# Kernel optimization log

Measured on AMD Instinct MI355X. Metric: run time of the kernel, lower is better.

Reference implementation:

```python
import jax, jax.numpy as jnp
import numpy as np

B, N, DIM, H = 8, 4096, 1024, 16
D = DIM // H
EPS_NORM = 1e-12
EPS_PI = 1e-8


def setup_inputs() -> dict:
    key = jax.random.key(0)
    k1, k2, k3 = jax.random.split(key, 3)
    x = jax.random.normal(k1, (B, N, DIM), dtype=jnp.float32)
    Wqkv = jax.random.normal(k2, (DIM, DIM), dtype=jnp.float32) * (1.0 / np.sqrt(DIM))
    temp = jnp.ones((H, 1), dtype=jnp.float32)
    Wout = jax.random.normal(k3, (DIM, DIM), dtype=jnp.float32) * (1.0 / np.sqrt(DIM))
    bout = jnp.zeros((DIM,), dtype=jnp.float32)
    return {"x": x, "Wqkv": Wqkv, "temp": temp, "Wout": Wout, "bout": bout}


def reference(x, Wqkv, temp, Wout, bout):
    b, n, dim = x.shape
    h, d = H, dim // H
    # qkv linear (no bias), then 'b n (h d) -> b h n d'
    w = (x @ Wqkv.T).reshape(b, n, h, d).transpose(0, 2, 1, 3)  # (b,h,N,d)
    # F.normalize along the sequence axis (dim=-2)
    norm = jnp.sqrt(jnp.sum(w * w, axis=-2, keepdims=True))
    w_normed = w / jnp.maximum(norm, EPS_NORM)
    # logits (b,h,N); temp (h,1) broadcasts over N. Softmax over dim=1 (heads).
    logits = jnp.sum(w_normed * w_normed, axis=-1) * temp[None, :, :]
    Pi = jax.nn.softmax(logits, axis=1)  # (b,h,N)
    Pi_norm = Pi / (jnp.sum(Pi, axis=-1, keepdims=True) + EPS_PI)
    # dots: (b,h,1,N) @ (b,h,N,d) -> (b,h,d)
    dots = jnp.einsum('bhn,bhnd->bhd', Pi_norm, w * w)
    attn = 1.0 / (1.0 + dots)  # (b,h,d)
    out = -(w * Pi[..., None]) * attn[:, :, None, :]  # (b,h,N,d)
    out = out.transpose(0, 2, 1, 3).reshape(b, n, dim)  # 'b h n d -> b n (h d)'
    return out @ Wout.T + bout
```

## Files before the change

### kernel.cpp

```cpp
#include <hip/hip_runtime.h>
#include <stdint.h>
#include <math.h>

#define B_ 8
#define N_ 4096
#define DIM_ 1024
#define H_ 16
#define M_ (B_*N_)

typedef unsigned short u16;
typedef __attribute__((ext_vector_type(8))) short bf16x8;
typedef __attribute__((ext_vector_type(4))) float f32x4;

__device__ __forceinline__ u16 f2bf(float f) {
    union { float f; uint32_t u; } c; c.f = f;
    uint32_t r = (c.u + 0x7fffu + ((c.u >> 16) & 1u)) >> 16;
    return (u16)r;
}
__device__ __forceinline__ float bf2f(u16 u) {
    union { uint32_t u; float f; } c; c.u = ((uint32_t)u) << 16;
    return c.f;
}
__device__ __forceinline__ void gload_lds16(const void* g, void* l) {
    __builtin_amdgcn_global_load_lds(
        (const __attribute__((address_space(1))) uint32_t*)g,
        (__attribute__((address_space(3))) uint32_t*)l, 16, 0, 0);
}

template<int MODE>
__global__ __launch_bounds__(512)
void gemm_mfma(const u16* __restrict__ Ah,
               const u16* __restrict__ Bh, const u16* __restrict__ Bl,
               const float* __restrict__ bias, float* __restrict__ Cf,
               float* __restrict__ norm2)
{
    __shared__ u16 sAh[256*32], sBh[128*32], sBl[128*32];
    __shared__ float cs[128];
    const int tid  = threadIdx.x;
    const int wid  = tid >> 6;
    const int lane = tid & 63;
    const int bid = blockIdx.x;
    const int lin = (bid & 7) * 128 + (bid >> 3);
    const int bx = lin & 7;
    const int by = lin >> 3;
    const int wm = wid >> 1, wn = wid & 1;
    const int fr = lane & 15;
    const int kb = (lane >> 4) * 8;

    f32x4 acc[4][4] = {};

    const int arow = by * 256;
    const int brow = bx * 128;

    for (int k0 = 0; k0 < DIM_; k0 += 32) {
        #pragma unroll
        for (int i = 0; i < 2; ++i) {
            const int chunk = i * 512 + tid;
            const int row   = chunk >> 2;
            const int ce    = (chunk & 3) * 8;
            const int soff  = i * 4096 + wid * 512;
            gload_lds16(Ah + (size_t)(arow + row) * DIM_ + k0 + ce, sAh + soff);
        }
        {
            const int row  = tid >> 2;
            const int ce   = (tid & 3) * 8;
            const int soff = wid * 512;
            gload_lds16(Bh + (size_t)(brow + row) * DIM_ + k0 + ce, sBh + soff);
            gload_lds16(Bl + (size_t)(brow + row) * DIM_ + k0 + ce, sBl + soff);
        }
        __syncthreads();

        bf16x8 a_[4], bh_[4], bl_[4];
        #pragma unroll
        for (int m = 0; m < 4; ++m) {
            const int r = wm * 64 + m * 16 + fr;
            a_[m] = *(const bf16x8*)(sAh + r * 32 + kb);
        }
        #pragma unroll
        for (int n = 0; n < 4; ++n) {
            const int c = wn * 64 + n * 16 + fr;
            bh_[n] = *(const bf16x8*)(sBh + c * 32 + kb);
            bl_[n] = *(const bf16x8*)(sBl + c * 32 + kb);
        }
        #pragma unroll
        for (int m = 0; m < 4; ++m)
            #pragma unroll
            for (int n = 0; n < 4; ++n)
                acc[m][n] = __builtin_amdgcn_mfma_f32_16x16x32_bf16(a_[m], bh_[n], acc[m][n], 0, 0, 0);
        #pragma unroll
        for (int m = 0; m < 4; ++m)
            #pragma unroll
            for (int n = 0; n < 4; ++n)
                acc[m][n] = __builtin_amdgcn_mfma_f32_16x16x32_bf16(a_[m], bl_[n], acc[m][n], 0, 0, 0);
        __syncthreads();
    }

    if (MODE == 1) {
        if (tid < 128) cs[tid] = 0.f;
        __syncthreads();
    }

    const int fq = lane >> 4;
    float csum[4] = {0.f, 0.f, 0.f, 0.f};
    #pragma unroll
    for (int m = 0; m < 4; ++m)
        #pragma unroll
        for (int n = 0; n < 4; ++n) {
            const int col  = bx * 128 + wn * 64 + n * 16 + fr;
            const int row0 = arow + wm * 64 + m * 16 + fq * 4;
            const float bv = (MODE == 0) ? bias[col] : 0.f;
            #pragma unroll
            for (int j = 0; j < 4; ++j) {
                const float v = acc[m][n][j];
                Cf[(size_t)(row0 + j) * DIM_ + col] = v + bv;
                if (MODE == 1) csum[n] = fmaf(v, v, csum[n]);
            }
        }

    if (MODE == 1) {
        #pragma unroll
        for (int n = 0; n < 4; ++n)
            atomicAdd(&cs[wn * 64 + n * 16 + fr], csum[n]);
        __syncthreads();
        const int b = arow >> 12;
        if (tid < 128) atomicAdd(&norm2[b * DIM_ + bx * 128 + tid], cs[tid]);
    }
}

__global__ __launch_bounds__(256)
void cvt_bf16(const float* __restrict__ src, u16* __restrict__ dh, int n4)
{
    const int i = blockIdx.x * 256 + threadIdx.x;
    if (i >= n4) return;
    const float4 v = ((const float4*)src)[i];
    ushort4 h;
    h.x = f2bf(v.x); h.y = f2bf(v.y); h.z = f2bf(v.z); h.w = f2bf(v.w);
    ((ushort4*)dh)[i] = h;
}

__global__ __launch_bounds__(256)
void split_f32(const float* __restrict__ src, u16* __restrict__ dh,
               u16* __restrict__ dl, int n4)
{
    const int i = blockIdx.x * 256 + threadIdx.x;
    if (i >= n4) return;
    const float4 v = ((const float4*)src)[i];
    ushort4 h, l;
    h.x = f2bf(v.x); l.x = f2bf(v.x - bf2f(h.x));
    h.y = f2bf(v.y); l.y = f2bf(v.y - bf2f(h.y));
    h.z = f2bf(v.z); l.z = f2bf(v.z - bf2f(h.z));
    h.w = f2bf(v.w); l.w = f2bf(v.w - bf2f(h.w));
    ((ushort4*)dh)[i] = h;
    ((ushort4*)dl)[i] = l;
}

__global__ __launch_bounds__(256)
void softmax_T(const float* __restrict__ w, const float* __restrict__ norm2,
               const float* __restrict__ temp, float* __restrict__ Pi,
               float* __restrict__ S, float* __restrict__ T)
{
    __shared__ float Tacc[4][1024];
    __shared__ float sS[H_];
    const int tid  = threadIdx.x;
    const int wv   = tid >> 6;
    const int lane = tid & 63;
    const int g    = lane >> 4;

    #pragma unroll
    for (int z = 0; z < 4; ++z)
        ((float4*)&Tacc[0][0])[z * 256 + tid] = float4{0.f, 0.f, 0.f, 0.f};
    if (tid < H_) sS[tid] = 0.f;
    __syncthreads();

    const int b = (blockIdx.x * 64) >> 12;
    float tl[4];
    float4 iv[4];
    #pragma unroll
    for (int rep = 0; rep < 4; ++rep) {
        tl[rep] = temp[rep * 4 + g];
        const int c = rep * 256 + lane * 4;
        const float4 nv = *(const float4*)(norm2 + (size_t)b * DIM_ + c);
        iv[rep].x = 1.0f / fmaxf(nv.x, 1e-24f);
        iv[rep].y = 1.0f / fmaxf(nv.y, 1e-24f);
        iv[rep].z = 1.0f / fmaxf(nv.z, 1e-24f);
        iv[rep].w = 1.0f / fmaxf(nv.w, 1e-24f);
    }

    float sSl[4] = {0.f, 0.f, 0.f, 0.f};

    for (int q = 0; q < 16; ++q) {
        const int r = blockIdx.x * 64 + wv * 16 + q;
        float4 wsq[4];
        float  l[4];
        #pragma unroll
        for (int rep = 0; rep < 4; ++rep) {
            const int c = rep * 256 + lane * 4;
            const float4 w4 = *(const float4*)(w + (size_t)r * DIM_ + c);
            wsq[rep].x = w4.x * w4.x; wsq[rep].y = w4.y * w4.y;
            wsq[rep].z = w4.z * w4.z; wsq[rep].w = w4.w * w4.w;
            l[rep] = wsq[rep].x * iv[rep].x + wsq[rep].y * iv[rep].y
                   + wsq[rep].z * iv[rep].z + wsq[rep].w * iv[rep].w;
        }
        #pragma unroll
        for (int off = 1; off < 16; off <<= 1)
            #pragma unroll
            for (int rep = 0; rep < 4; ++rep) l[rep] += __shfl_xor(l[rep], off, 64);
        #pragma unroll
        for (int rep = 0; rep < 4; ++rep) l[rep] *= tl[rep];

        float m = fmaxf(fmaxf(l[0], l[1]), fmaxf(l[2], l[3]));
        m = fmaxf(m, __shfl_xor(m, 16, 64));
        m = fmaxf(m, __shfl_xor(m, 32, 64));
        float e[4], s = 0.f;
        #pragma unroll
        for (int rep = 0; rep < 4; ++rep) { e[rep] = expf(l[rep] - m); s += e[rep]; }
        s += __shfl_xor(s, 16, 64);
        s += __shfl_xor(s, 32, 64);
        const float inv_s = 1.0f / s;

        float pi[4];
        #pragma unroll
        for (int rep = 0; rep < 4; ++rep) pi[rep] = e[rep] * inv_s;

        #pragma unroll
        for (int rep = 0; rep < 4; ++rep) {
            const int c = rep * 256 + lane * 4;
            float4* t = (float4*)&Tacc[wv][c];
            float4 tv = *t;
            tv.x = fmaf(pi[rep], wsq[rep].x, tv.x);
            tv.y = fmaf(pi[rep], wsq[rep].y, tv.y);
            tv.z = fmaf(pi[rep], wsq[rep].z, tv.z);
            tv.w = fmaf(pi[rep], wsq[rep].w, tv.w);
            *t = tv;
        }

        if ((lane & 15) == 0) {
            #pragma unroll
            for (int rep = 0; rep < 4; ++rep) {
                Pi[(size_t)r * H_ + rep * 4 + g] = pi[rep];
                sSl[rep] += pi[rep];
            }
        }
    }

    if ((lane & 15) == 0) {
        #pragma unroll
        for (int rep = 0; rep < 4; ++rep) atomicAdd(&sS[rep * 4 + g], sSl[rep]);
    }
    __syncthreads();
    if (tid < H_) atomicAdd(&S[b * H_ + tid], sS[tid]);
    #pragma unroll
    for (int z = 0; z < 4; ++z) {
        const int c = z * 256 + tid;
        const float t = Tacc[0][c] + Tacc[1][c] + Tacc[2][c] + Tacc[3][c];
        atomicAdd(&T[b * DIM_ + c], t);
    }
}

__global__ __launch_bounds__(256)
void split_scaled(const float* __restrict__ w, const float* __restrict__ Pi,
                  const float* __restrict__ S, const float* __restrict__ T,
                  u16* __restrict__ ah)
{
    const int i = blockIdx.x * 256 + threadIdx.x;
    const int r = i >> 8;
    const int c = (i & 255) * 4;
    const int b = r >> 12;
    const int h = c >> 6;
    const float p  = -Pi[(size_t)r * H_ + h];
    const float Sv = S[b * H_ + h] + 1e-8f;
    const float4 T4 = *(const float4*)(T + b * DIM_ + c);
    const float4 w4 = ((const float4*)w)[i];
    ushort4 oh;
    oh.x = f2bf(w4.x * p / (1.0f + T4.x / Sv));
    oh.y = f2bf(w4.y * p / (1.0f + T4.y / Sv));
    oh.z = f2bf(w4.z * p / (1.0f + T4.z / Sv));
    oh.w = f2bf(w4.w * p / (1.0f + T4.w / Sv));
    ((ushort4*)ah)[i] = oh;
}

template<bool FUSE>
__global__ __launch_bounds__(256, 4)
void gemm128(const float* __restrict__ A, const float* __restrict__ Bw,
             const float* __restrict__ bias, float* __restrict__ C,
             const float* __restrict__ Pi, const float* __restrict__ attn)
{
    __shared__ float As[16][128];
    __shared__ float Bs[16][128];
    const int tid  = threadIdx.x;
    const int bx   = blockIdx.x;
    const int by   = blockIdx.y;
    const int lrow = tid >> 2;
    const int lk   = (tid & 3) << 2;
    const int tx   = tid & 15;
    const int ty   = tid >> 4;
    const size_t K = DIM_;
    const float* Ap = A  + (size_t)(by * 128 + lrow) * K + lk;
    const float* Bp = Bw + (size_t)(bx * 128 + lrow) * K + lk;

    float acc[8][8];
    #pragma unroll
    for (int i = 0; i < 8; ++i)
        #pragma unroll
        for (int j = 0; j < 8; ++j) acc[i][j] = 0.f;

    for (int k0 = 0; k0 < DIM_; k0 += 16) {
        float4 a0 = *(const float4*)(Ap + k0);
        float4 a1 = *(const float4*)(Ap + k0 + (size_t)64 * K);
        float4 b0 = *(const float4*)(Bp + k0);
        float4 b1 = *(const float4*)(Bp + k0 + (size_t)64 * K);
        if (FUSE) {
            const int r0 = by * 128 + lrow;
            const int c  = k0 + lk;
            const int b  = r0 >> 12;
            const float4 at = *(const float4*)(attn + b * DIM_ + c);
            const float p0 = -Pi[(size_t)r0 * H_ + (c >> 6)];
            const float p1 = -Pi[(size_t)(r0 + 64) * H_ + (c >> 6)];
            a0.x *= p0 * at.x; a0.y *= p0 * at.y; a0.z *= p0 * at.z; a0.w *= p0 * at.w;
            a1.x *= p1 * at.x; a1.y *= p1 * at.y; a1.z *= p1 * at.z; a1.w *= p1 * at.w;
        }
        __syncthreads();
        As[lk + 0][lrow]      = a0.x; As[lk + 1][lrow]      = a0.y;
        As[lk + 2][lrow]      = a0.z; As[lk + 3][lrow]      = a0.w;
        As[lk + 0][lrow + 64] = a1.x; As[lk + 1][lrow + 64] = a1.y;
        As[lk + 2][lrow + 64] = a1.z; As[lk + 3][lrow + 64] = a1.w;
        Bs[lk + 0][lrow]      = b0.x; Bs[lk + 1][lrow]      = b0.y;
        Bs[lk + 2][lrow]      = b0.z; Bs[lk + 3][lrow]      = b0.w;
        Bs[lk + 0][lrow + 64] = b1.x; Bs[lk + 1][lrow + 64] = b1.y;
        Bs[lk + 2][lrow + 64] = b1.z; Bs[lk + 3][lrow + 64] = b1.w;
        __syncthreads();
        #pragma unroll
        for (int kk = 0; kk < 16; ++kk) {
            const float4 av0 = *(const float4*)&As[kk][ty * 4];
            const float4 av1 = *(const float4*)&As[kk][ty * 4 + 64];
            const float4 bv0 = *(const float4*)&Bs[kk][tx * 4];
            const float4 bv1 = *(const float4*)&Bs[kk][tx * 4 + 64];
            const float a[8] = {av0.x, av0.y, av0.z, av0.w, av1.x, av1.y, av1.z, av1.w};
            const float b[8] = {bv0.x, bv0.y, bv0.z, bv0.w, bv1.x, bv1.y, bv1.z, bv1.w};
            #pragma unroll
            for (int i = 0; i < 8; ++i)
                #pragma unroll
                for (int j = 0; j < 8; ++j)
                    acc[i][j] = fmaf(a[i], b[j], acc[i][j]);
        }
    }
    #pragma unroll
    for (int i = 0; i < 8; ++i) {
        const int r = by * 128 + ((i < 4) ? (ty * 4 + i) : (64 + ty * 4 + (i - 4)));
        #pragma unroll
        for (int jb = 0; jb < 2; ++jb) {
            const int c0 = bx * 128 + (jb ? (64 + tx * 4) : (tx * 4));
            float4 v;
            v.x = acc[i][jb * 4 + 0]; v.y = acc[i][jb * 4 + 1];
            v.z = acc[i][jb * 4 + 2]; v.w = acc[i][jb * 4 + 3];
            if (bias) {
                const float4 bv = *(const float4*)(bias + c0);
                v.x += bv.x; v.y += bv.y; v.z += bv.z; v.w += bv.w;
            }
            *(float4*)(C + (size_t)r * DIM_ + c0) = v;
        }
    }
}

__global__ __launch_bounds__(256)
void colsum_sq_f32(const float* __restrict__ w, float* __restrict__ norm2)
{
    const int c  = blockIdx.x * 256 + threadIdx.x;
    const int b  = blockIdx.z;
    const int n0 = blockIdx.y * (N_ / 16);
    const float* p = w + (size_t)(b * N_ + n0) * DIM_ + c;
    float s = 0.f;
    for (int n = 0; n < N_ / 16; ++n) {
        const float v = p[(size_t)n * DIM_];
        s = fmaf(v, v, s);
    }
    atomicAdd(&norm2[b * DIM_ + c], s);
}

__global__ void finalize_inv(float* __restrict__ norm2)
{
    const int i = blockIdx.x * 256 + threadIdx.x;
    norm2[i] = 1.0f / fmaxf(norm2[i], 1e-24f);
}

__global__ __launch_bounds__(256)
void softmax_heads_f32(const float* __restrict__ w, const float* __restrict__ inv2,
                       const float* __restrict__ temp, float* __restrict__ Pi,
                       float* __restrict__ S)
{
    __shared__ float sS[H_];
    const int tid = threadIdx.x;
    if (tid < H_) sS[tid] = 0.f;
    __syncthreads();
    const int wv   = tid >> 6;
    const int lane = tid & 63;
    const int r    = blockIdx.x * 4 + wv;
    const int b    = r >> 12;
    const int g    = lane >> 4;
    float l[4];
    #pragma unroll
    for (int rep = 0; rep < 4; ++rep) {
        const int c = rep * 256 + lane * 4;
        const float4 wv4 = *(const float4*)(w    + (size_t)r * DIM_ + c);
        const float4 iv4 = *(const float4*)(inv2 + (size_t)b * DIM_ + c);
        l[rep] = wv4.x * wv4.x * iv4.x + wv4.y * wv4.y * iv4.y
               + wv4.z * wv4.z * iv4.z + wv4.w * wv4.w * iv4.w;
    }
    #pragma unroll
    for (int off = 1; off < 16; off <<= 1)
        #pragma unroll
        for (int rep = 0; rep < 4; ++rep) l[rep] += __shfl_xor(l[rep], off, 64);
    #pragma unroll
    for (int rep = 0; rep < 4; ++rep) l[rep] *= temp[rep * 4 + g];
    float m = fmaxf(fmaxf(l[0], l[1]), fmaxf(l[2], l[3]));
    m = fmaxf(m, __shfl_xor(m, 16, 64));
    m = fmaxf(m, __shfl_xor(m, 32, 64));
    float e[4], s = 0.f;
    #pragma unroll
    for (int rep = 0; rep < 4; ++rep) { e[rep] = expf(l[rep] - m); s += e[rep]; }
    s += __shfl_xor(s, 16, 64);
    s += __shfl_xor(s, 32, 64);
    const float inv_s = 1.0f / s;
    if ((lane & 15) == 0) {
        #pragma unroll
        for (int rep = 0; rep < 4; ++rep) {
            const float pi = e[rep] * inv_s;
            Pi[(size_t)r * H_ + rep * 4 + g] = pi;
            atomicAdd(&sS[rep * 4 + g], pi);
        }
    }
    __syncthreads();
    if (tid < H_) atomicAdd(&S[b * H_ + tid], sS[tid]);
}

__global__ __launch_bounds__(256)
void colsum_T_f32(const float* __restrict__ w, const float* __restrict__ Pi,
                  float* __restrict__ T)
{
    const int c  = blockIdx.x * 256 + threadIdx.x;
    const int b  = blockIdx.z;
    const int n0 = blockIdx.y * (N_ / 16);
    const int h  = c >> 6;
    const float* p  = w  + (size_t)(b * N_ + n0) * DIM_ + c;
    const float* pp = Pi + (size_t)(b * N_ + n0) * H_ + h;
    float s = 0.f;
    for (int n = 0; n < N_ / 16; ++n) {
        const float v = p[(size_t)n * DIM_];
        s = fmaf(pp[(size_t)n * H_] * v, v, s);
    }
    atomicAdd(&T[b * DIM_ + c], s);
}

__global__ void finalize_attn(const float* __restrict__ T, const float* __restrict__ S,
                              float* __restrict__ attn)
{
    const int i = blockIdx.x * 256 + threadIdx.x;
    const int b = i >> 10;
    const int c = i & 1023;
    const float dots = T[i] / (S[b * H_ + (c >> 6)] + 1e-8f);
    attn[i] = 1.0f / (1.0f + dots);
}

extern "C" void kernel_launch(void* const* d_in, const int* in_sizes, int n_in,
                              void* d_out, int out_size, void* d_ws, size_t ws_size,
                              hipStream_t stream)
{
    const float* x    = (const float*)d_in[0];
    const float* Wqkv = (const float*)d_in[1];
    const float* temp = (const float*)d_in[2];
    const float* Wout = (const float*)d_in[3];
    const float* bout = (const float*)d_in[4];
    float* out = (float*)d_out;

    const size_t MD = (size_t)M_ * DIM_;
    const size_t DD = (size_t)DIM_ * DIM_;
    const size_t NEED_MFMA = MD * 2
                           + MD * 4
                           + 4 * DD * 2
                           + (size_t)M_ * H_ * 4
                           + (size_t)(8192 + 128 + 8192) * 4 + 4096;

    if (ws_size >= NEED_MFMA) {
        uint8_t* p = (uint8_t*)d_ws;
        u16* xh = (u16*)p; p += MD * 2;
        float* w = (float*)p; p += MD * 4;
        u16* qh = (u16*)p; p += DD * 2;
        u16* ql = (u16*)p; p += DD * 2;
        u16* oh = (u16*)p; p += DD * 2;
        u16* ol = (u16*)p; p += DD * 2;
        float* Pi    = (float*)p; p += (size_t)M_ * H_ * 4;
        float* norm2 = (float*)p; p += 8192 * 4;
        float* S     = (float*)p; p += 128 * 4;
        float* T     = (float*)p;

        hipMemsetAsync(norm2, 0, (size_t)(8192 + 128 + 8192) * 4, stream);

        cvt_bf16<<<(int)(MD / 4 / 256), 256, 0, stream>>>(x, xh, (int)(MD / 4));
        split_f32<<<(int)(DD / 4 / 256), 256, 0, stream>>>(Wqkv, qh, ql, (int)(DD / 4));
        split_f32<<<(int)(DD / 4 / 256), 256, 0, stream>>>(Wout, oh, ol, (int)(DD / 4));

        gemm_mfma<1><<<1024, 512, 0, stream>>>(xh, qh, ql, nullptr, w, norm2);

        softmax_T<<<M_ / 64, 256, 0, stream>>>(w, norm2, temp, Pi, S, T);

        split_scaled<<<(int)(MD / 4 / 256), 256, 0, stream>>>(w, Pi, S, T, xh);

        gemm_mfma<0><<<1024, 512, 0, stream>>>(xh, oh, ol, bout, out, nullptr);
    } else {
        float* ws    = (float*)d_ws;
        float* w     = ws;
        float* Pi    = w + MD;
        float* norm2 = Pi + (size_t)M_ * H_;
        float* S     = norm2 + 8192;
        float* T     = S + 128;
        float* attnv = T + 8192;

        hipMemsetAsync(norm2, 0, (size_t)(8192 + 128 + 8192) * 4, stream);

        gemm128<false><<<dim3(8, 256), 256, 0, stream>>>(x, Wqkv, nullptr, w, nullptr, nullptr);
        colsum_sq_f32<<<dim3(4, 16, 8), 256, 0, stream>>>(w, norm2);
        finalize_inv<<<32, 256, 0, stream>>>(norm2);
        softmax_heads_f32<<<M_ / 4, 256, 0, stream>>>(w, norm2, temp, Pi, S);
        colsum_T_f32<<<dim3(4, 16, 8), 256, 0, stream>>>(w, Pi, T);
        finalize_attn<<<32, 256, 0, stream>>>(T, S, attnv);
        gemm128<true><<<dim3(8, 256), 256, 0, stream>>>(w, Wout, bout, out, Pi, attnv);
    }
}
```

Before: 537.6 us.

## Fuse fp32-to-bf16 conversion and attention scaling into MFMA GEMM A-tile loads

Both MFMA GEMMs now read the fp32 activation directly and convert it to bf16 in registers before writing a swizzled LDS tile. For the output GEMM the Pi and attention scaling is applied in the same step. This removes the separate cvt_bf16 and split_scaled passes and the bf16 intermediate buffer. The weight splits and the stats memset are merged into one prep kernel. In exchange the A tile now goes through registers rather than direct global-to-LDS loads, and the GEMM re-reads Pi for every tile, which may reduce load/compute overlap. Rounding switches to a cheaper round-half-up conversion.

```diff
diff --git a/kernel.cpp b/kernel.cpp
--- a/kernel.cpp
+++ b/kernel.cpp
@@ -17,6 +17,10 @@
     uint32_t r = (c.u + 0x7fffu + ((c.u >> 16) & 1u)) >> 16;
     return (u16)r;
 }
+__device__ __forceinline__ u16 f2bf_fast(float f) {
+    union { float f; uint32_t u; } c; c.f = f;
+    return (u16)((c.u + 0x8000u) >> 16);
+}
 __device__ __forceinline__ float bf2f(u16 u) {
     union { uint32_t u; float f; } c; c.u = ((uint32_t)u) << 16;
     return c.f;
@@ -29,12 +33,16 @@
 
 template<int MODE>
 __global__ __launch_bounds__(512)
-void gemm_mfma(const u16* __restrict__ Ah,
+void gemm_mfma(const float* __restrict__ Asrc,
                const u16* __restrict__ Bh, const u16* __restrict__ Bl,
                const float* __restrict__ bias, float* __restrict__ Cf,
-               float* __restrict__ norm2)
-{
-    __shared__ u16 sAh[256*32], sBh[128*32], sBl[128*32];
+               float* __restrict__ norm2,
+               const float* __restrict__ Pi, const float* __restrict__ Sg,
+               const float* __restrict__ Tg)
+{
+    __shared__ u16 sA[256*32];
+    __shared__ u16 sBh[128*32], sBl[128*32];
+    __shared__ float atn[DIM_];
     __shared__ float cs[128];
     const int tid  = threadIdx.x;
     const int wid  = tid >> 6;
@@ -47,20 +55,25 @@
     const int fr = lane & 15;
     const int kb = (lane >> 4) * 8;
 
-    f32x4 acc[4][4] = {};
-
     const int arow = by * 256;
     const int brow = bx * 128;
+    const int bb   = arow >> 12;
+
+    if (MODE == 0) {
+        for (int c = tid; c < DIM_; c += 512) {
+            const float Sv = Sg[bb * H_ + (c >> 6)] + 1e-8f;
+            atn[c] = Sv / (Sv + Tg[bb * DIM_ + c]);
+        }
+        __syncthreads();
+    }
+
+    f32x4 acc[4][4] = {};
+
+    const int ar = (tid >> 3);
+    const int c4 = (tid & 7) * 4;
+    const int sw = ((ar & 3) << 3);
 
     for (int k0 = 0; k0 < DIM_; k0 += 32) {
-        #pragma unroll
-        for (int i = 0; i < 2; ++i) {
-            const int chunk = i * 512 + tid;
-            const int row   = chunk >> 2;
-            const int ce    = (chunk & 3) * 8;
-            const int soff  = i * 4096 + wid * 512;
-            gload_lds16(Ah + (size_t)(arow + row) * DIM_ + k0 + ce, sAh + soff);
-        }
         {
             const int row  = tid >> 2;
             const int ce   = (tid & 3) * 8;
@@ -68,13 +81,34 @@
             gload_lds16(Bh + (size_t)(brow + row) * DIM_ + k0 + ce, sBh + soff);
             gload_lds16(Bl + (size_t)(brow + row) * DIM_ + k0 + ce, sBl + soff);
         }
+        ushort4 av[4];
+        #pragma unroll
+        for (int i = 0; i < 4; ++i) {
+            const int r = i * 64 + ar;
+            const float4 v = *(const float4*)(Asrc + (size_t)(arow + r) * DIM_ + k0 + c4);
+            float s0, s1, s2, s3;
+            if (MODE == 0) {
+                const int c = k0 + c4;
+                const float p = -Pi[(size_t)(arow + r) * H_ + (c >> 6)];
+                const float4 a4 = *(const float4*)&atn[c];
+                s0 = v.x * p * a4.x; s1 = v.y * p * a4.y;
+                s2 = v.z * p * a4.z; s3 = v.w * p * a4.w;
+            } else { s0 = v.x; s1 = v.y; s2 = v.z; s3 = v.w; }
+            av[i].x = f2bf_fast(s0); av[i].y = f2bf_fast(s1);
+            av[i].z = f2bf_fast(s2); av[i].w = f2bf_fast(s3);
+        }
+        #pragma unroll
+        for (int i = 0; i < 4; ++i) {
+            const int r = i * 64 + ar;
+            *(ushort4*)(sA + r * 32 + (c4 ^ sw)) = av[i];
+        }
         __syncthreads();
 
         bf16x8 a_[4], bh_[4], bl_[4];
         #pragma unroll
         for (int m = 0; m < 4; ++m) {
             const int r = wm * 64 + m * 16 + fr;
-            a_[m] = *(const bf16x8*)(sAh + r * 32 + kb);
+            a_[m] = *(const bf16x8*)(sA + r * 32 + (kb ^ ((r & 3) << 3)));
         }
         #pragma unroll
         for (int n = 0; n < 4; ++n) {
@@ -122,36 +156,36 @@
         for (int n = 0; n < 4; ++n)
             atomicAdd(&cs[wn * 64 + n * 16 + fr], csum[n]);
         __syncthreads();
-        const int b = arow >> 12;
-        if (tid < 128) atomicAdd(&norm2[b * DIM_ + bx * 128 + tid], cs[tid]);
+        if (tid < 128) atomicAdd(&norm2[bb * DIM_ + bx * 128 + tid], cs[tid]);
     }
 }
 
 __global__ __launch_bounds__(256)
-void cvt_bf16(const float* __restrict__ src, u16* __restrict__ dh, int n4)
+void prep(const float* __restrict__ Wqkv, const float* __restrict__ Wout,
+          u16* __restrict__ qh, u16* __restrict__ ql,
+          u16* __restrict__ oh, u16* __restrict__ ol,
+          float* __restrict__ stats)
 {
     const int i = blockIdx.x * 256 + threadIdx.x;
-    if (i >= n4) return;
-    const float4 v = ((const float4*)src)[i];
-    ushort4 h;
-    h.x = f2bf(v.x); h.y = f2bf(v.y); h.z = f2bf(v.z); h.w = f2bf(v.w);
-    ((ushort4*)dh)[i] = h;
-}
-
-__global__ __launch_bounds__(256)
-void split_f32(const float* __restrict__ src, u16* __restrict__ dh,
-               u16* __restrict__ dl, int n4)
-{
-    const int i = blockIdx.x * 256 + threadIdx.x;
-    if (i >= n4) return;
-    const float4 v = ((const float4*)src)[i];
-    ushort4 h, l;
-    h.x = f2bf(v.x); l.x = f2bf(v.x - bf2f(h.x));
-    h.y = f2bf(v.y); l.y = f2bf(v.y - bf2f(h.y));
-    h.z = f2bf(v.z); l.z = f2bf(v.z - bf2f(h.z));
-    h.w = f2bf(v.w); l.w = f2bf(v.w - bf2f(h.w));
-    ((ushort4*)dh)[i] = h;
-    ((ushort4*)dl)[i] = l;
+    {
+        const float4 v = ((const float4*)Wqkv)[i];
+        ushort4 h, l;
+        h.x = f2bf(v.x); l.x = f2bf(v.x - bf2f(h.x));
+        h.y = f2bf(v.y); l.y = f2bf(v.y - bf2f(h.y));
+        h.z = f2bf(v.z); l.z = f2bf(v.z - bf2f(h.z));
+        h.w = f2bf(v.w); l.w = f2bf(v.w - bf2f(h.w));
+        ((ushort4*)qh)[i] = h; ((ushort4*)ql)[i] = l;
+    }
+    {
+        const float4 v = ((const float4*)Wout)[i];
+        ushort4 h, l;
+        h.x = f2bf(v.x); l.x = f2bf(v.x - bf2f(h.x));
+        h.y = f2bf(v.y); l.y = f2bf(v.y - bf2f(h.y));
+        h.z = f2bf(v.z); l.z = f2bf(v.z - bf2f(h.z));
+        h.w = f2bf(v.w); l.w = f2bf(v.w - bf2f(h.w));
+        ((ushort4*)oh)[i] = h; ((ushort4*)ol)[i] = l;
+    }
+    if (i < 8192 + 128 + 8192) stats[i] = 0.f;
 }
 
 __global__ __launch_bounds__(256)
@@ -255,28 +289,6 @@
         const float t = Tacc[0][c] + Tacc[1][c] + Tacc[2][c] + Tacc[3][c];
         atomicAdd(&T[b * DIM_ + c], t);
     }
-}
-
-__global__ __launch_bounds__(256)
-void split_scaled(const float* __restrict__ w, const float* __restrict__ Pi,
-                  const float* __restrict__ S, const float* __restrict__ T,
-                  u16* __restrict__ ah)
-{
-    const int i = blockIdx.x * 256 + threadIdx.x;
-    const int r = i >> 8;
-    const int c = (i & 255) * 4;
-    const int b = r >> 12;
-    const int h = c >> 6;
-    const float p  = -Pi[(size_t)r * H_ + h];
-    const float Sv = S[b * H_ + h] + 1e-8f;
-    const float4 T4 = *(const float4*)(T + b * DIM_ + c);
-    const float4 w4 = ((const float4*)w)[i];
-    ushort4 oh;
-    oh.x = f2bf(w4.x * p / (1.0f + T4.x / Sv));
-    oh.y = f2bf(w4.y * p / (1.0f + T4.y / Sv));
-    oh.z = f2bf(w4.z * p / (1.0f + T4.z / Sv));
-    oh.w = f2bf(w4.w * p / (1.0f + T4.w / Sv));
-    ((ushort4*)ah)[i] = oh;
 }
 
 template<bool FUSE>
@@ -474,15 +486,13 @@
 
     const size_t MD = (size_t)M_ * DIM_;
     const size_t DD = (size_t)DIM_ * DIM_;
-    const size_t NEED_MFMA = MD * 2
-                           + MD * 4
+    const size_t NEED_MFMA = MD * 4
                            + 4 * DD * 2
                            + (size_t)M_ * H_ * 4
                            + (size_t)(8192 + 128 + 8192) * 4 + 4096;
 
     if (ws_size >= NEED_MFMA) {
         uint8_t* p = (uint8_t*)d_ws;
-        u16* xh = (u16*)p; p += MD * 2;
         float* w = (float*)p; p += MD * 4;
         u16* qh = (u16*)p; p += DD * 2;
         u16* ql = (u16*)p; p += DD * 2;
@@ -493,19 +503,15 @@
         float* S     = (float*)p; p += 128 * 4;
         float* T     = (float*)p;
 
-        hipMemsetAsync(norm2, 0, (size_t)(8192 + 128 + 8192) * 4, stream);
-
-        cvt_bf16<<<(int)(MD / 4 / 256), 256, 0, stream>>>(x, xh, (int)(MD / 4));
-        split_f32<<<(int)(DD / 4 / 256), 256, 0, stream>>>(Wqkv, qh, ql, (int)(DD / 4));
-        split_f32<<<(int)(DD / 4 / 256), 256, 0, stream>>>(Wout, oh, ol, (int)(DD / 4));
-
-        gemm_mfma<1><<<1024, 512, 0, stream>>>(xh, qh, ql, nullptr, w, norm2);
+        prep<<<1024, 256, 0, stream>>>(Wqkv, Wout, qh, ql, oh, ol, norm2);
+
+        gemm_mfma<1><<<1024, 512, 0, stream>>>(x, qh, ql, nullptr, w, norm2,
+                                               nullptr, nullptr, nullptr);
 
         softmax_T<<<M_ / 64, 256, 0, stream>>>(w, norm2, temp, Pi, S, T);
 
-        split_scaled<<<(int)(MD / 4 / 256), 256, 0, stream>>>(w, Pi, S, T, xh);
-
-        gemm_mfma<0><<<1024, 512, 0, stream>>>(xh, oh, ol, bout, out, nullptr);
+        gemm_mfma<0><<<1024, 512, 0, stream>>>(w, oh, ol, bout, out, nullptr,
+                                               Pi, S, T);
     } else {
         float* ws    = (float*)d_ws;
         float* w     = ws;
```

New measurement: 651.3 us. 21.2% more time.
